# Kernel optimization log

Hardware: AMD Instinct MI355X
Metric: run time of the kernel (lower is better)

## Reference

```python
import jax, jax.numpy as jnp
import numpy as np

N = 100000      # nodes
F_IN = 256      # num_node_features
E = 1600000     # edges (before self-loops)
DIMS = [F_IN, 128, 100, 32, 2]  # GCNConv layer widths


def _glorot(key, fan_in, fan_out):
    s = jnp.sqrt(6.0 / (fan_in + fan_out))
    return jax.random.uniform(key, (fan_in, fan_out), jnp.float32, -s, s)


def setup_inputs() -> dict:
    key = jax.random.key(0)
    ks = jax.random.split(key, 10)
    x = jax.random.normal(ks[0], (N, F_IN), jnp.float32)
    edge_index = jax.random.randint(ks[1], (2, E), 0, N, jnp.int32)
    inp = {"x": x, "edge_index": edge_index}
    for i in range(4):
        inp[f"W{i+1}"] = _glorot(ks[2 + 2 * i], DIMS[i], DIMS[i + 1])
        inp[f"b{i+1}"] = jnp.zeros((DIMS[i + 1],), jnp.float32)
    return inp


def reference(x, edge_index, W1, b1, W2, b2, W3, b3, W4, b4):
    n = x.shape[0]
    loops = jnp.arange(n, dtype=edge_index.dtype)
    src = jnp.concatenate([edge_index[0], loops])  # [E+N]
    dst = jnp.concatenate([edge_index[1], loops])
    # symmetric normalization: deg^-1/2[src] * deg^-1/2[dst] (self-loops included)
    deg = jax.ops.segment_sum(jnp.ones_like(src, x.dtype), dst, num_segments=n)
    dis = jax.lax.rsqrt(jnp.maximum(deg, 1.0))
    norm = (dis[src] * dis[dst])[:, None]  # [E+N, 1]

    def conv(h, W, b):
        h = h @ W                                      # [N, out]
        msg = h[src] * norm                            # gather + scale [E+N, out]
        return jax.ops.segment_sum(msg, dst, num_segments=n) + b

    h = jax.nn.leaky_relu(conv(x, W1, b1), negative_slope=0.1)
    h = jax.nn.leaky_relu(conv(h, W2, b2), negative_slope=0.1)
    h = jax.nn.leaky_relu(conv(h, W3, b3), negative_slope=0.1)
    h = conv(h, W4, b4)
    return jax.nn.softmax(h, axis=-1)
```

## Files before the change

kernel.cpp:

```cpp
#include <hip/hip_runtime.h>
#include <math.h>


typedef unsigned short ushort_t;
typedef unsigned int   uint_t;
typedef short  bf16x8 __attribute__((ext_vector_type(8)));
typedef float  f32x4  __attribute__((ext_vector_type(4)));

#define BKT_SHIFT 8
#define BKT_CAP   5120
#define BIN_CHUNK 4096

__device__ __forceinline__ ushort_t f2bf(float f) {
    union { float f; uint_t u; } v; v.f = f;
    uint_t u = v.u;
    u += 0x7fffu + ((u >> 16) & 1u);
    return (ushort_t)(u >> 16);
}
__device__ __forceinline__ float bflo(uint_t u) {
    union { uint_t q; float f; } v; v.q = u << 16; return v.f;
}
__device__ __forceinline__ float bfhi(uint_t u) {
    union { uint_t q; float f; } v; v.q = u & 0xffff0000u; return v.f;
}


__global__ __launch_bounds__(256) void bin_kernel(const int* __restrict__ srcArr,
                                                  const int* __restrict__ dstArr,
                                                  int* __restrict__ bkt_cursor,
                                                  uint2* __restrict__ staging,
                                                  int E, int nb) {
    __shared__ int hist[512];
    __shared__ int base[512];
    for (int b = threadIdx.x; b < 512; b += 256) hist[b] = 0;
    __syncthreads();
    const int e0 = blockIdx.x * BIN_CHUNK;
    #pragma unroll 4
    for (int k = 0; k < BIN_CHUNK / 256; ++k) {
        int e = e0 + k * 256 + threadIdx.x;
        if (e < E) atomicAdd(&hist[dstArr[e] >> BKT_SHIFT], 1);
    }
    __syncthreads();
    for (int b = threadIdx.x; b < nb; b += 256) {
        int h = hist[b];
        base[b] = h ? atomicAdd(&bkt_cursor[b], h) : 0;
    }
    __syncthreads();
    for (int b = threadIdx.x; b < 512; b += 256) hist[b] = 0;
    __syncthreads();
    #pragma unroll 4
    for (int k = 0; k < BIN_CHUNK / 256; ++k) {
        int e = e0 + k * 256 + threadIdx.x;
        if (e < E) {
            int s = srcArr[e], d = dstArr[e];
            int b = d >> BKT_SHIFT;
            int p = atomicAdd(&hist[b], 1);
            int idx = base[b] + p;
            if (idx < BKT_CAP)
                staging[(size_t)b * BKT_CAP + idx] = make_uint2((uint_t)s, (uint_t)d);
        }
    }
}

__global__ __launch_bounds__(256) void deg_from_staging_kernel(const uint2* __restrict__ staging,
                                                               const int* __restrict__ bkt_cursor,
                                                               int* __restrict__ degi,
                                                               float* __restrict__ dis, int n) {
    __shared__ int cur[256];
    const int b  = blockIdx.x;
    const int lo = b << BKT_SHIFT;
    const int nl = min(256, n - lo);
    cur[threadIdx.x] = 0;
    __syncthreads();
    int cnt = min(bkt_cursor[b], BKT_CAP);
    for (int e = threadIdx.x; e < cnt; e += 256) {
        uint2 p = staging[(size_t)b * BKT_CAP + e];
        atomicAdd(&cur[(int)p.y - lo], 1);
    }
    __syncthreads();
    if ((int)threadIdx.x < nl) {
        int d = cur[threadIdx.x];
        degi[lo + threadIdx.x] = d;
        dis[lo + threadIdx.x] = rsqrtf((float)(d + 1));
    }
}

__global__ void scan_block_kernel(const int* __restrict__ degi, int* __restrict__ row_excl,
                                  int* __restrict__ bsums, int n) {
    __shared__ int buf[1024];
    int i = blockIdx.x * 1024 + threadIdx.x;
    int v = (i < n) ? degi[i] : 0;
    buf[threadIdx.x] = v;
    __syncthreads();
    for (int off = 1; off < 1024; off <<= 1) {
        int t = (threadIdx.x >= (unsigned)off) ? buf[threadIdx.x - off] : 0;
        __syncthreads();
        buf[threadIdx.x] += t;
        __syncthreads();
    }
    if (i < n) row_excl[i] = buf[threadIdx.x] - v;
    if (threadIdx.x == 1023) bsums[blockIdx.x] = buf[1023];
}

__global__ void scan_sums_kernel(int* __restrict__ bsums, int nb) {
    __shared__ int buf[128];
    int v = ((int)threadIdx.x < nb) ? bsums[threadIdx.x] : 0;
    buf[threadIdx.x] = v;
    __syncthreads();
    for (int off = 1; off < 128; off <<= 1) {
        int t = (threadIdx.x >= (unsigned)off) ? buf[threadIdx.x - off] : 0;
        __syncthreads();
        buf[threadIdx.x] += t;
        __syncthreads();
    }
    if ((int)threadIdx.x < nb) bsums[threadIdx.x] = buf[threadIdx.x] - v;
    if (threadIdx.x == 0) bsums[nb] = buf[127];
}

__global__ void scan_add_kernel(int* __restrict__ row_start, const int* __restrict__ bsums,
                                int n, int nb) {
    int i = blockIdx.x * blockDim.x + threadIdx.x;
    if (i < n) row_start[i] += bsums[i >> 10];
    else if (i == n) row_start[n] = bsums[nb];
}

__global__ __launch_bounds__(256) void csr_build_kernel(const uint2* __restrict__ staging,
                                                        const int* __restrict__ bkt_cursor,
                                                        const int* __restrict__ row_start,
                                                        int* __restrict__ csr_src, int n) {
    __shared__ int rs[257];
    __shared__ int cur[256];
    __shared__ int seg[BKT_CAP];
    const int b  = blockIdx.x;
    const int lo = b << BKT_SHIFT;
    const int nl = min(256, n - lo);
    if ((int)threadIdx.x <= nl) rs[threadIdx.x] = row_start[lo + threadIdx.x];
    cur[threadIdx.x] = 0;
    __syncthreads();
    const int sbase = rs[0];
    int cnt = min(bkt_cursor[b], BKT_CAP);
    for (int e = threadIdx.x; e < cnt; e += 256) {
        uint2 p = staging[(size_t)b * BKT_CAP + e];
        int ln = (int)p.y - lo;
        int q  = atomicAdd(&cur[ln], 1);
        seg[(rs[ln] - sbase) + q] = (int)p.x;
    }
    __syncthreads();
    for (int i = threadIdx.x; i < cnt; i += 256) csr_src[sbase + i] = seg[i];
}

__global__ void wt_all_kernel(const float* __restrict__ W1, const float* __restrict__ W2,
                              const float* __restrict__ W3,
                              ushort_t* __restrict__ Wt1, ushort_t* __restrict__ Wt2,
                              ushort_t* __restrict__ Wt3) {
    int idx = blockIdx.x * blockDim.x + threadIdx.x;
    if (idx < 32768) {
        int nn = idx >> 8, k = idx & 255;
        Wt1[idx] = f2bf(W1[(size_t)k * 128 + nn]);
    } else if (idx < 49152) {
        int j = idx - 32768;
        int nn = j >> 7, k = j & 127;
        float v = (nn < 100) ? W2[(size_t)k * 100 + nn] : 0.f;
        Wt2[j] = f2bf(v);
    } else if (idx < 57344) {
        int j = idx - 49152;
        int nn = j >> 7, k = j & 127;
        float v = (k < 100 && nn < 32) ? W3[(size_t)k * 32 + nn] : 0.f;
        Wt3[j] = f2bf(v);
    }
}

template <bool A_FP32, int NFR>
__global__ __launch_bounds__(256) void mfma_gemm(const void* __restrict__ Av,
                                                 const ushort_t* __restrict__ Bt,
                                                 ushort_t* __restrict__ C,
                                                 const float* __restrict__ dis,
                                                 int M, int K, int lda, int ldb,
                                                 int ldc, int nstore) {
    constexpr int BN = NFR * 32;
    __shared__ __attribute__((aligned(16))) ushort_t As[128][72];
    __shared__ __attribute__((aligned(16))) ushort_t Bs[BN][72];

    const int t    = threadIdx.x;
    const int lane = t & 63;
    const int w    = t >> 6;
    const int wm   = w >> 1, wn = w & 1;
    const int m0   = blockIdx.x * 128;
    const int n0   = blockIdx.y * BN;

    f32x4 acc[4][NFR];
    #pragma unroll
    for (int mi = 0; mi < 4; ++mi)
        #pragma unroll
        for (int ni = 0; ni < NFR; ++ni) acc[mi][ni] = (f32x4){0.f, 0.f, 0.f, 0.f};

    const int srow = t >> 3;
    const int scol = (t & 7) * 8;

    for (int k0 = 0; k0 < K; k0 += 64) {
        #pragma unroll
        for (int it = 0; it < 4; ++it) {
            int r = srow + it * 32;
            int gm = m0 + r;
            bf16x8 v = {0, 0, 0, 0, 0, 0, 0, 0};
            if (gm < M) {
                if (A_FP32) {
                    const float* A = (const float*)Av;
                    const float4 f0 = *(const float4*)(A + (size_t)gm * lda + k0 + scol);
                    const float4 f1 = *(const float4*)(A + (size_t)gm * lda + k0 + scol + 4);
                    ushort_t o[8] = { f2bf(f0.x), f2bf(f0.y), f2bf(f0.z), f2bf(f0.w),
                                      f2bf(f1.x), f2bf(f1.y), f2bf(f1.z), f2bf(f1.w) };
                    v = *(const bf16x8*)o;
                } else {
                    const ushort_t* A = (const ushort_t*)Av;
                    v = *(const bf16x8*)(A + (size_t)gm * lda + k0 + scol);
                }
            }
            *(bf16x8*)&As[r][scol] = v;
        }
        #pragma unroll
        for (int it = 0; it < BN / 32; ++it) {
            int r = srow + it * 32;
            bf16x8 v = *(const bf16x8*)(Bt + (size_t)(n0 + r) * ldb + k0 + scol);
            *(bf16x8*)&Bs[r][scol] = v;
        }
        __syncthreads();
        #pragma unroll
        for (int kk = 0; kk < 2; ++kk) {
            bf16x8 af[4], bfr[NFR];
            const int kc = kk * 32 + (lane >> 4) * 8;
            #pragma unroll
            for (int mi = 0; mi < 4; ++mi)
                af[mi] = *(const bf16x8*)&As[wm * 64 + mi * 16 + (lane & 15)][kc];
            #pragma unroll
            for (int ni = 0; ni < NFR; ++ni)
                bfr[ni] = *(const bf16x8*)&Bs[wn * (BN / 2) + ni * 16 + (lane & 15)][kc];
            #pragma unroll
            for (int mi = 0; mi < 4; ++mi)
                #pragma unroll
                for (int ni = 0; ni < NFR; ++ni)
                    acc[mi][ni] = __builtin_amdgcn_mfma_f32_16x16x32_bf16(
                        af[mi], bfr[ni], acc[mi][ni], 0, 0, 0);
        }
        __syncthreads();
    }

    #pragma unroll
    for (int mi = 0; mi < 4; ++mi)
        #pragma unroll
        for (int r = 0; r < 4; ++r) {
            int gm = m0 + wm * 64 + mi * 16 + (lane >> 4) * 4 + r;
            if (gm >= M) continue;
            float d = dis[gm];
            #pragma unroll
            for (int ni = 0; ni < NFR; ++ni) {
                int gn = n0 + wn * (BN / 2) + ni * 16 + (lane & 15);
                if (gn < nstore)
                    C[(size_t)gm * ldc + gn] = f2bf(acc[mi][ni][r] * d);
            }
        }
}

template <int F>
__global__ void aggregate128_kernel(const ushort_t* __restrict__ h, const int* __restrict__ row_start,
                                    const int* __restrict__ csr_src,
                                    const float* __restrict__ dis, const float* __restrict__ bias,
                                    ushort_t* __restrict__ out, int n) {
    int wid  = threadIdx.x >> 6;
    int lane = threadIdx.x & 63;
    int node = blockIdx.x * 4 + wid;
    if (node >= n) return;
    const int q  = lane >> 4;
    const int fb = (lane & 15) * 8;
    float a[8];
    #pragma unroll
    for (int j = 0; j < 8; ++j) a[j] = 0.f;

    int i = row_start[node], end = row_start[node + 1];

#define ACC8(U)                                                     \
    do {                                                            \
        a[0] += bflo((U).x); a[1] += bfhi((U).x);                   \
        a[2] += bflo((U).y); a[3] += bfhi((U).y);                   \
        a[4] += bflo((U).z); a[5] += bfhi((U).z);                   \
        a[6] += bflo((U).w); a[7] += bfhi((U).w);                   \
    } while (0)

    #pragma unroll 2
    for (; i + 8 <= end; i += 8) {
        int sA = csr_src[i + q];
        int sB = csr_src[i + 4 + q];
        uint4 u = *(const uint4*)(h + (size_t)sA * 128 + fb);
        uint4 v = *(const uint4*)(h + (size_t)sB * 128 + fb);
        ACC8(u);
        ACC8(v);
    }
    int r = end - i;
    if (r > 0) {
        if (q < r) {
            int sA = csr_src[i + q];
            uint4 u = *(const uint4*)(h + (size_t)sA * 128 + fb);
            ACC8(u);
        }
        if (q + 4 < r) {
            int sB = csr_src[i + 4 + q];
            uint4 v = *(const uint4*)(h + (size_t)sB * 128 + fb);
            ACC8(v);
        }
    }
#undef ACC8

    #pragma unroll
    for (int j = 0; j < 8; ++j) {
        a[j] += __shfl_xor(a[j], 16);
        a[j] += __shfl_xor(a[j], 32);
    }

    if (q == 0) {
        uint4 su = *(const uint4*)(h + (size_t)node * 128 + fb);
        a[0] += bflo(su.x); a[1] += bfhi(su.x);
        a[2] += bflo(su.y); a[3] += bfhi(su.y);
        a[4] += bflo(su.z); a[5] += bfhi(su.z);
        a[6] += bflo(su.w); a[7] += bfhi(su.w);
        float dn = dis[node];
        #pragma unroll
        for (int j = 0; j < 8; ++j) {
            float b = (fb + j < F) ? bias[fb + j] : 0.f;
            float v = a[j] * dn + b;
            v = (v > 0.f) ? v : 0.1f * v;
            if (fb + j >= F) v = 0.f;
            a[j] = v;
        }
        uint4 o;
        o.x = (uint_t)f2bf(a[0]) | ((uint_t)f2bf(a[1]) << 16);
        o.y = (uint_t)f2bf(a[2]) | ((uint_t)f2bf(a[3]) << 16);
        o.z = (uint_t)f2bf(a[4]) | ((uint_t)f2bf(a[5]) << 16);
        o.w = (uint_t)f2bf(a[6]) | ((uint_t)f2bf(a[7]) << 16);
        *(uint4*)(out + (size_t)node * 128 + fb) = o;
    }
}

__global__ void aggregate32_kernel(const ushort_t* __restrict__ h, const int* __restrict__ row_start,
                                   const int* __restrict__ csr_src,
                                   const float* __restrict__ dis, const float* __restrict__ bias,
                                   ushort_t* __restrict__ out, int n) {
    int lane16 = threadIdx.x & 15;
    int node = blockIdx.x * (blockDim.x >> 4) + (threadIdx.x >> 4);
    if (node >= n) return;
    const int f0 = 2 * lane16;
    uint_t v = *(const uint_t*)(h + (size_t)node * 32 + f0);
    float acc0 = bflo(v);
    float acc1 = bfhi(v);
    int i = row_start[node], end = row_start[node + 1];
    for (; i + 4 <= end; i += 4) {
        int s0 = csr_src[i], s1 = csr_src[i + 1], s2 = csr_src[i + 2], s3 = csr_src[i + 3];
        uint_t u0 = *(const uint_t*)(h + (size_t)s0 * 32 + f0);
        uint_t u1 = *(const uint_t*)(h + (size_t)s1 * 32 + f0);
        uint_t u2 = *(const uint_t*)(h + (size_t)s2 * 32 + f0);
        uint_t u3 = *(const uint_t*)(h + (size_t)s3 * 32 + f0);
        acc0 += bflo(u0) + bflo(u1) + bflo(u2) + bflo(u3);
        acc1 += bfhi(u0) + bfhi(u1) + bfhi(u2) + bfhi(u3);
    }
    for (; i < end; ++i) {
        int s = csr_src[i];
        uint_t u = *(const uint_t*)(h + (size_t)s * 32 + f0);
        acc0 += bflo(u); acc1 += bfhi(u);
    }
    float dn = dis[node];
    acc0 = acc0 * dn + bias[f0];
    acc1 = acc1 * dn + bias[f0 + 1];
    acc0 = (acc0 > 0.f) ? acc0 : 0.1f * acc0;
    acc1 = (acc1 > 0.f) ? acc1 : 0.1f * acc1;
    uint_t o = (uint_t)f2bf(acc0) | ((uint_t)f2bf(acc1) << 16);
    *(uint_t*)(out + (size_t)node * 32 + f0) = o;
}

__global__ void gemm32x2_kernel(const ushort_t* __restrict__ H, const float* __restrict__ W4,
                                const float* __restrict__ dis, float* __restrict__ C, int n) {
    int node = blockIdx.x * blockDim.x + threadIdx.x;
    if (node >= n) return;
    const uint_t* row = (const uint_t*)(H + (size_t)node * 32);
    float a0 = 0.f, a1 = 0.f;
    #pragma unroll
    for (int k2 = 0; k2 < 16; ++k2) {
        uint_t u = row[k2];
        float x0 = bflo(u), x1 = bfhi(u);
        int k = 2 * k2;
        a0 += x0 * W4[k * 2]     + x1 * W4[(k + 1) * 2];
        a1 += x0 * W4[k * 2 + 1] + x1 * W4[(k + 1) * 2 + 1];
    }
    float d = dis[node];
    C[2 * (size_t)node]     = a0 * d;
    C[2 * (size_t)node + 1] = a1 * d;
}

__global__ void aggregate2_softmax_kernel(const float* __restrict__ h, const int* __restrict__ row_start,
                                          const int* __restrict__ csr_src,
                                          const float* __restrict__ dis, const float* __restrict__ bias,
                                          float* __restrict__ out, int n) {
    int node = blockIdx.x * blockDim.x + threadIdx.x;
    if (node >= n) return;
    float a0 = h[2 * (size_t)node];
    float a1 = h[2 * (size_t)node + 1];
    int beg = row_start[node], end = row_start[node + 1];
    for (int i = beg; i < end; ++i) {
        int s = csr_src[i];
        a0 += h[2 * (size_t)s];
        a1 += h[2 * (size_t)s + 1];
    }
    float dn = dis[node];
    a0 = a0 * dn + bias[0];
    a1 = a1 * dn + bias[1];
    float m  = fmaxf(a0, a1);
    float e0 = expf(a0 - m), e1 = expf(a1 - m);
    float inv = 1.f / (e0 + e1);
    out[2 * (size_t)node]     = e0 * inv;
    out[2 * (size_t)node + 1] = e1 * inv;
}


extern "C" void kernel_launch(void* const* d_in, const int* in_sizes, int n_in,
                              void* d_out, int out_size, void* d_ws, size_t ws_size,
                              hipStream_t stream) {
    const float* x  = (const float*)d_in[0];
    const int*   ei = (const int*)d_in[1];
    const float* W1 = (const float*)d_in[2];
    const float* b1 = (const float*)d_in[3];
    const float* W2 = (const float*)d_in[4];
    const float* b2 = (const float*)d_in[5];
    const float* W3 = (const float*)d_in[6];
    const float* b3 = (const float*)d_in[7];
    const float* W4 = (const float*)d_in[8];
    const float* b4 = (const float*)d_in[9];

    const int N = in_sizes[0] / 256;
    const int E = in_sizes[1] / 2;
    const int* srcA = ei;
    const int* dstA = ei + E;
    const int nbkt = (N + 255) >> BKT_SHIFT;

    char* ws = (char*)d_ws;
    size_t off = 0;
    auto alloc = [&](size_t bytes) {
        void* p = ws + off;
        off = (off + bytes + 255) & ~(size_t)255;
        return p;
    };
    int*      degi       = (int*)alloc((size_t)N * 4);
    float*    dis        = (float*)alloc((size_t)N * 4);
    int*      row_start  = (int*)alloc((size_t)(N + 1) * 4);
    int*      bsums      = (int*)alloc(512 * 4);
    int*      bkt_cursor = (int*)alloc((size_t)nbkt * 4);
    int*      csr_src    = (int*)alloc((size_t)E * 4);
    uint2*    staging    = (uint2*)alloc((size_t)nbkt * BKT_CAP * 8);
    ushort_t* bufA       = (ushort_t*)alloc((size_t)N * 128 * 2);
    ushort_t* bufB       = (ushort_t*)alloc((size_t)N * 128 * 2);
    float*    C4         = (float*)alloc((size_t)N * 2 * 4);
    ushort_t* Wt1        = (ushort_t*)alloc((size_t)128 * 256 * 2);
    ushort_t* Wt2        = (ushort_t*)alloc((size_t)128 * 128 * 2);
    ushort_t* Wt3        = (ushort_t*)alloc((size_t)64 * 128 * 2);
    (void)ws_size;

    hipMemsetAsync(bkt_cursor, 0, (size_t)nbkt * 4, stream);

    bin_kernel<<<(E + BIN_CHUNK - 1) / BIN_CHUNK, 256, 0, stream>>>(
        srcA, dstA, bkt_cursor, staging, E, nbkt);
    deg_from_staging_kernel<<<nbkt, 256, 0, stream>>>(staging, bkt_cursor, degi, dis, N);
    const int nb = (N + 1023) >> 10;
    scan_block_kernel<<<nb, 1024, 0, stream>>>(degi, row_start, bsums, N);
    scan_sums_kernel<<<1, 128, 0, stream>>>(bsums, nb);
    scan_add_kernel<<<(N + 256) / 256, 256, 0, stream>>>(row_start, bsums, N, nb);
    csr_build_kernel<<<nbkt, 256, 0, stream>>>(staging, bkt_cursor, row_start, csr_src, N);

    wt_all_kernel<<<(57344 + 255) / 256, 256, 0, stream>>>(W1, W2, W3, Wt1, Wt2, Wt3);

    const int gx = (N + 127) / 128;
    const int aggBlocks128 = (N + 3) / 4;
    const int aggBlocks32  = (N + 15) / 16;

    mfma_gemm<true, 4><<<dim3(gx, 1), 256, 0, stream>>>(x, Wt1, bufA, dis, N, 256, 256, 256, 128, 128);
    aggregate128_kernel<128><<<aggBlocks128, 256, 0, stream>>>(
        bufA, row_start, csr_src, dis, b1, bufB, N);
    mfma_gemm<false, 4><<<dim3(gx, 1), 256, 0, stream>>>(bufB, Wt2, bufA, dis, N, 128, 128, 128, 128, 128);
    aggregate128_kernel<100><<<aggBlocks128, 256, 0, stream>>>(
        bufA, row_start, csr_src, dis, b2, bufB, N);
    mfma_gemm<false, 2><<<dim3(gx, 1), 256, 0, stream>>>(bufB, Wt3, bufA, dis, N, 128, 128, 128, 32, 32);
    aggregate32_kernel<<<aggBlocks32, 256, 0, stream>>>(
        bufA, row_start, csr_src, dis, b3, bufB, N);
    gemm32x2_kernel<<<(N + 255) / 256, 256, 0, stream>>>(bufB, W4, dis, C4, N);
    aggregate2_softmax_kernel<<<(N + 255) / 256, 256, 0, stream>>>(
        C4, row_start, csr_src, dis, b4, (float*)d_out, N);
}
```

Baseline: 321.7 us.

## Replace LDS-tiled MFMA GEMM with direct-register GEMM without shared memory

The shared-memory tiled GEMM is replaced by a kernel in which each wave loads its A rows and all of B straight from global memory into MFMA operand registers. Each wave owns 32 rows and the full output width, with the K loop fully unrolled at compile time. This removes LDS staging and the two __syncthreads per K step. In exchange, B (the small weight matrix) is re-read from global or cache by every wave, and the A loads are strided rather than coalesced through LDS.

```diff
diff --git a/kernel.cpp b/kernel.cpp
--- a/kernel.cpp
+++ b/kernel.cpp
@@ -170,91 +170,72 @@
     }
 }
 
-template <bool A_FP32, int NFR>
-__global__ __launch_bounds__(256) void mfma_gemm(const void* __restrict__ Av,
-                                                 const ushort_t* __restrict__ Bt,
-                                                 ushort_t* __restrict__ C,
-                                                 const float* __restrict__ dis,
-                                                 int M, int K, int lda, int ldb,
-                                                 int ldc, int nstore) {
-    constexpr int BN = NFR * 32;
-    __shared__ __attribute__((aligned(16))) ushort_t As[128][72];
-    __shared__ __attribute__((aligned(16))) ushort_t Bs[BN][72];
-
-    const int t    = threadIdx.x;
-    const int lane = t & 63;
-    const int w    = t >> 6;
-    const int wm   = w >> 1, wn = w & 1;
-    const int m0   = blockIdx.x * 128;
-    const int n0   = blockIdx.y * BN;
-
-    f32x4 acc[4][NFR];
-    #pragma unroll
-    for (int mi = 0; mi < 4; ++mi)
+template <bool A_FP32, int NFR, int KT>
+__global__ __launch_bounds__(256) void gemm_direct(const void* __restrict__ Av,
+                                                   const ushort_t* __restrict__ Bt,
+                                                   ushort_t* __restrict__ C,
+                                                   const float* __restrict__ dis,
+                                                   int M, int lda, int ldb,
+                                                   int ldc, int nstore) {
+    const int lane = threadIdx.x & 63;
+    const int w    = threadIdx.x >> 6;
+    const int row0 = blockIdx.x * 128 + w * 32;
+    const int rsel = lane & 15;
+    const int kq   = (lane >> 4) * 8;
+
+    f32x4 acc[2][NFR];
+    #pragma unroll
+    for (int mi = 0; mi < 2; ++mi)
         #pragma unroll
         for (int ni = 0; ni < NFR; ++ni) acc[mi][ni] = (f32x4){0.f, 0.f, 0.f, 0.f};
 
-    const int srow = t >> 3;
-    const int scol = (t & 7) * 8;
-
-    for (int k0 = 0; k0 < K; k0 += 64) {
-        #pragma unroll
-        for (int it = 0; it < 4; ++it) {
-            int r = srow + it * 32;
-            int gm = m0 + r;
+    const int gm0 = row0 + rsel;
+    const int gm1 = row0 + 16 + rsel;
+
+    #pragma unroll
+    for (int k0 = 0; k0 < KT; k0 += 32) {
+        bf16x8 af[2];
+        #pragma unroll
+        for (int mi = 0; mi < 2; ++mi) {
+            int gm = mi ? gm1 : gm0;
             bf16x8 v = {0, 0, 0, 0, 0, 0, 0, 0};
             if (gm < M) {
                 if (A_FP32) {
                     const float* A = (const float*)Av;
-                    const float4 f0 = *(const float4*)(A + (size_t)gm * lda + k0 + scol);
-                    const float4 f1 = *(const float4*)(A + (size_t)gm * lda + k0 + scol + 4);
+                    const float4 f0 = *(const float4*)(A + (size_t)gm * lda + k0 + kq);
+                    const float4 f1 = *(const float4*)(A + (size_t)gm * lda + k0 + kq + 4);
                     ushort_t o[8] = { f2bf(f0.x), f2bf(f0.y), f2bf(f0.z), f2bf(f0.w),
                                       f2bf(f1.x), f2bf(f1.y), f2bf(f1.z), f2bf(f1.w) };
                     v = *(const bf16x8*)o;
                 } else {
                     const ushort_t* A = (const ushort_t*)Av;
-                    v = *(const bf16x8*)(A + (size_t)gm * lda + k0 + scol);
+                    v = *(const bf16x8*)(A + (size_t)gm * lda + k0 + kq);
                 }
             }
-            *(bf16x8*)&As[r][scol] = v;
-        }
-        #pragma unroll
-        for (int it = 0; it < BN / 32; ++it) {
-            int r = srow + it * 32;
-            bf16x8 v = *(const bf16x8*)(Bt + (size_t)(n0 + r) * ldb + k0 + scol);
-            *(bf16x8*)&Bs[r][scol] = v;
-        }
-        __syncthreads();
-        #pragma unroll
-        for (int kk = 0; kk < 2; ++kk) {
-            bf16x8 af[4], bfr[NFR];
-            const int kc = kk * 32 + (lane >> 4) * 8;
-            #pragma unroll
-            for (int mi = 0; mi < 4; ++mi)
-                af[mi] = *(const bf16x8*)&As[wm * 64 + mi * 16 + (lane & 15)][kc];
+            af[mi] = v;
+        }
+        bf16x8 bfr[NFR];
+        #pragma unroll
+        for (int ni = 0; ni < NFR; ++ni)
+            bfr[ni] = *(const bf16x8*)(Bt + (size_t)(ni * 16 + rsel) * ldb + k0 + kq);
+        #pragma unroll
+        for (int mi = 0; mi < 2; ++mi)
             #pragma unroll
             for (int ni = 0; ni < NFR; ++ni)
-                bfr[ni] = *(const bf16x8*)&Bs[wn * (BN / 2) + ni * 16 + (lane & 15)][kc];
-            #pragma unroll
-            for (int mi = 0; mi < 4; ++mi)
-                #pragma unroll
-                for (int ni = 0; ni < NFR; ++ni)
-                    acc[mi][ni] = __builtin_amdgcn_mfma_f32_16x16x32_bf16(
-                        af[mi], bfr[ni], acc[mi][ni], 0, 0, 0);
-        }
-        __syncthreads();
-    }
-
-    #pragma unroll
-    for (int mi = 0; mi < 4; ++mi)
+                acc[mi][ni] = __builtin_amdgcn_mfma_f32_16x16x32_bf16(
+                    af[mi], bfr[ni], acc[mi][ni], 0, 0, 0);
+    }
+
+    #pragma unroll
+    for (int mi = 0; mi < 2; ++mi)
         #pragma unroll
         for (int r = 0; r < 4; ++r) {
-            int gm = m0 + wm * 64 + mi * 16 + (lane >> 4) * 4 + r;
+            int gm = row0 + mi * 16 + (lane >> 4) * 4 + r;
             if (gm >= M) continue;
             float d = dis[gm];
             #pragma unroll
             for (int ni = 0; ni < NFR; ++ni) {
-                int gn = n0 + wn * (BN / 2) + ni * 16 + (lane & 15);
+                int gn = ni * 16 + rsel;
                 if (gn < nstore)
                     C[(size_t)gm * ldc + gn] = f2bf(acc[mi][ni][r] * d);
             }
@@ -478,13 +459,13 @@
     const int aggBlocks128 = (N + 3) / 4;
     const int aggBlocks32  = (N + 15) / 16;
 
-    mfma_gemm<true, 4><<<dim3(gx, 1), 256, 0, stream>>>(x, Wt1, bufA, dis, N, 256, 256, 256, 128, 128);
+    gemm_direct<true, 8, 256><<<gx, 256, 0, stream>>>(x, Wt1, bufA, dis, N, 256, 256, 128, 128);
     aggregate128_kernel<128><<<aggBlocks128, 256, 0, stream>>>(
         bufA, row_start, csr_src, dis, b1, bufB, N);
-    mfma_gemm<false, 4><<<dim3(gx, 1), 256, 0, stream>>>(bufB, Wt2, bufA, dis, N, 128, 128, 128, 128, 128);
+    gemm_direct<false, 8, 128><<<gx, 256, 0, stream>>>(bufB, Wt2, bufA, dis, N, 128, 128, 128, 128);
     aggregate128_kernel<100><<<aggBlocks128, 256, 0, stream>>>(
         bufA, row_start, csr_src, dis, b2, bufB, N);
-    mfma_gemm<false, 2><<<dim3(gx, 1), 256, 0, stream>>>(bufB, Wt3, bufA, dis, N, 128, 128, 128, 32, 32);
+    gemm_direct<false, 2, 128><<<gx, 256, 0, stream>>>(bufB, Wt3, bufA, dis, N, 128, 128, 32, 32);
     aggregate32_kernel<<<aggBlocks32, 256, 0, stream>>>(
         bufA, row_start, csr_src, dis, b3, bufB, N);
     gemm32x2_kernel<<<(N + 255) / 256, 256, 0, stream>>>(bufB, W4, dis, C4, N);
```

After: 350.8 us. 1.09x slower.

## Pre-cast x to bf16, shrink GEMM M-tile, swap MFMA operands for vector stores

Applied to the files above, without the earlier changes.

Adds a separate kernel that casts the fp32 input features to a bf16 buffer before the first GEMM, so the GEMM no longer converts on load. The GEMM M-tile is halved from 128 to 64 rows, which doubles the block count and lowers register use. The MFMA operands are swapped so each lane holds four consecutive output columns and can write them as one packed 8-byte store. The third layer now uses a 32-wide tile instead of 64. The cost is an extra pass over x, reading 100 MB of fp32 and writing 50 MB of bf16, plus a larger workspace.

```diff
diff --git a/kernel.cpp b/kernel.cpp
--- a/kernel.cpp
+++ b/kernel.cpp
@@ -147,6 +147,20 @@
     }
     __syncthreads();
     for (int i = threadIdx.x; i < cnt; i += 256) csr_src[sbase + i] = seg[i];
+}
+
+
+__global__ void cast_bf16_kernel(const float* __restrict__ in, ushort_t* __restrict__ out, int n8) {
+    int i = blockIdx.x * blockDim.x + threadIdx.x;
+    if (i >= n8) return;
+    const float4 f0 = ((const float4*)in)[2 * i];
+    const float4 f1 = ((const float4*)in)[2 * i + 1];
+    uint4 o;
+    o.x = (uint_t)f2bf(f0.x) | ((uint_t)f2bf(f0.y) << 16);
+    o.y = (uint_t)f2bf(f0.z) | ((uint_t)f2bf(f0.w) << 16);
+    o.z = (uint_t)f2bf(f1.x) | ((uint_t)f2bf(f1.y) << 16);
+    o.w = (uint_t)f2bf(f1.z) | ((uint_t)f2bf(f1.w) << 16);
+    ((uint4*)out)[i] = o;
 }
 
 __global__ void wt_all_kernel(const float* __restrict__ W1, const float* __restrict__ W2,
@@ -170,27 +184,27 @@
     }
 }
 
-template <bool A_FP32, int NFR>
-__global__ __launch_bounds__(256) void mfma_gemm(const void* __restrict__ Av,
+template <int NFR>
+__global__ __launch_bounds__(256) void gemm_tile(const ushort_t* __restrict__ A,
                                                  const ushort_t* __restrict__ Bt,
                                                  ushort_t* __restrict__ C,
                                                  const float* __restrict__ dis,
-                                                 int M, int K, int lda, int ldb,
-                                                 int ldc, int nstore) {
+                                                 int M, int K, int lda, int ldb, int ldc) {
     constexpr int BN = NFR * 32;
-    __shared__ __attribute__((aligned(16))) ushort_t As[128][72];
+    __shared__ __attribute__((aligned(16))) ushort_t As[64][72];
     __shared__ __attribute__((aligned(16))) ushort_t Bs[BN][72];
 
     const int t    = threadIdx.x;
     const int lane = t & 63;
     const int w    = t >> 6;
     const int wm   = w >> 1, wn = w & 1;
-    const int m0   = blockIdx.x * 128;
-    const int n0   = blockIdx.y * BN;
-
-    f32x4 acc[4][NFR];
+    const int m0   = blockIdx.x * 64;
+    const int rsel = lane & 15;
+    const int q    = lane >> 4;
+
+    f32x4 acc[2][NFR];
     #pragma unroll
-    for (int mi = 0; mi < 4; ++mi)
+    for (int mi = 0; mi < 2; ++mi)
         #pragma unroll
         for (int ni = 0; ni < NFR; ++ni) acc[mi][ni] = (f32x4){0.f, 0.f, 0.f, 0.f};
 
@@ -199,66 +213,53 @@
 
     for (int k0 = 0; k0 < K; k0 += 64) {
         #pragma unroll
-        for (int it = 0; it < 4; ++it) {
+        for (int it = 0; it < 2; ++it) {
             int r = srow + it * 32;
             int gm = m0 + r;
             bf16x8 v = {0, 0, 0, 0, 0, 0, 0, 0};
-            if (gm < M) {
-                if (A_FP32) {
-                    const float* A = (const float*)Av;
-                    const float4 f0 = *(const float4*)(A + (size_t)gm * lda + k0 + scol);
-                    const float4 f1 = *(const float4*)(A + (size_t)gm * lda + k0 + scol + 4);
-                    ushort_t o[8] = { f2bf(f0.x), f2bf(f0.y), f2bf(f0.z), f2bf(f0.w),
-                                      f2bf(f1.x), f2bf(f1.y), f2bf(f1.z), f2bf(f1.w) };
-                    v = *(const bf16x8*)o;
-                } else {
-                    const ushort_t* A = (const ushort_t*)Av;
-                    v = *(const bf16x8*)(A + (size_t)gm * lda + k0 + scol);
-                }
-            }
+            if (gm < M) v = *(const bf16x8*)(A + (size_t)gm * lda + k0 + scol);
             *(bf16x8*)&As[r][scol] = v;
         }
         #pragma unroll
         for (int it = 0; it < BN / 32; ++it) {
             int r = srow + it * 32;
-            bf16x8 v = *(const bf16x8*)(Bt + (size_t)(n0 + r) * ldb + k0 + scol);
+            bf16x8 v = *(const bf16x8*)(Bt + (size_t)r * ldb + k0 + scol);
             *(bf16x8*)&Bs[r][scol] = v;
         }
         __syncthreads();
         #pragma unroll
-        for (int kk = 0; kk < 2; ++kk) {
-            bf16x8 af[4], bfr[NFR];
-            const int kc = kk * 32 + (lane >> 4) * 8;
+        for (int ks = 0; ks < 2; ++ks) {
+            const int kc = ks * 32 + q * 8;
+            bf16x8 af[2], bfr[NFR];
             #pragma unroll
-            for (int mi = 0; mi < 4; ++mi)
-                af[mi] = *(const bf16x8*)&As[wm * 64 + mi * 16 + (lane & 15)][kc];
+            for (int mi = 0; mi < 2; ++mi)
+                af[mi] = *(const bf16x8*)&As[wm * 32 + mi * 16 + rsel][kc];
             #pragma unroll
             for (int ni = 0; ni < NFR; ++ni)
-                bfr[ni] = *(const bf16x8*)&Bs[wn * (BN / 2) + ni * 16 + (lane & 15)][kc];
+                bfr[ni] = *(const bf16x8*)&Bs[wn * (BN / 2) + ni * 16 + rsel][kc];
             #pragma unroll
-            for (int mi = 0; mi < 4; ++mi)
+            for (int mi = 0; mi < 2; ++mi)
                 #pragma unroll
                 for (int ni = 0; ni < NFR; ++ni)
                     acc[mi][ni] = __builtin_amdgcn_mfma_f32_16x16x32_bf16(
-                        af[mi], bfr[ni], acc[mi][ni], 0, 0, 0);
+                        bfr[ni], af[mi], acc[mi][ni], 0, 0, 0);
         }
         __syncthreads();
     }
 
     #pragma unroll
-    for (int mi = 0; mi < 4; ++mi)
-        #pragma unroll
-        for (int r = 0; r < 4; ++r) {
-            int gm = m0 + wm * 64 + mi * 16 + (lane >> 4) * 4 + r;
-            if (gm >= M) continue;
-            float d = dis[gm];
-            #pragma unroll
-            for (int ni = 0; ni < NFR; ++ni) {
-                int gn = n0 + wn * (BN / 2) + ni * 16 + (lane & 15);
-                if (gn < nstore)
-                    C[(size_t)gm * ldc + gn] = f2bf(acc[mi][ni][r] * d);
-            }
-        }
+    for (int mi = 0; mi < 2; ++mi) {
+        const int gm = m0 + wm * 32 + mi * 16 + rsel;
+        if (gm >= M) continue;
+        const float d = dis[gm];
+        #pragma unroll
+        for (int ni = 0; ni < NFR; ++ni) {
+            uint2 o;
+            o.x = (uint_t)f2bf(acc[mi][ni][0] * d) | ((uint_t)f2bf(acc[mi][ni][1] * d) << 16);
+            o.y = (uint_t)f2bf(acc[mi][ni][2] * d) | ((uint_t)f2bf(acc[mi][ni][3] * d) << 16);
+            *(uint2*)(C + (size_t)gm * ldc + wn * (BN / 2) + ni * 16 + q * 4) = o;
+        }
+    }
 }
 
 template <int F>
@@ -453,6 +454,7 @@
     int*      bkt_cursor = (int*)alloc((size_t)nbkt * 4);
     int*      csr_src    = (int*)alloc((size_t)E * 4);
     uint2*    staging    = (uint2*)alloc((size_t)nbkt * BKT_CAP * 8);
+    ushort_t* xb         = (ushort_t*)alloc((size_t)N * 256 * 2);
     ushort_t* bufA       = (ushort_t*)alloc((size_t)N * 128 * 2);
     ushort_t* bufB       = (ushort_t*)alloc((size_t)N * 128 * 2);
     float*    C4         = (float*)alloc((size_t)N * 2 * 4);
@@ -473,18 +475,20 @@
     csr_build_kernel<<<nbkt, 256, 0, stream>>>(staging, bkt_cursor, row_start, csr_src, N);
 
     wt_all_kernel<<<(57344 + 255) / 256, 256, 0, stream>>>(W1, W2, W3, Wt1, Wt2, Wt3);
-
-    const int gx = (N + 127) / 128;
+    const int n8 = N * 32;
+    cast_bf16_kernel<<<(n8 + 255) / 256, 256, 0, stream>>>(x, xb, n8);
+
+    const int gx = (N + 63) / 64;
     const int aggBlocks128 = (N + 3) / 4;
     const int aggBlocks32  = (N + 15) / 16;
 
-    mfma_gemm<true, 4><<<dim3(gx, 1), 256, 0, stream>>>(x, Wt1, bufA, dis, N, 256, 256, 256, 128, 128);
+    gemm_tile<4><<<gx, 256, 0, stream>>>(xb, Wt1, bufA, dis, N, 256, 256, 256, 128);
     aggregate128_kernel<128><<<aggBlocks128, 256, 0, stream>>>(
         bufA, row_start, csr_src, dis, b1, bufB, N);
-    mfma_gemm<false, 4><<<dim3(gx, 1), 256, 0, stream>>>(bufB, Wt2, bufA, dis, N, 128, 128, 128, 128, 128);
+    gemm_tile<4><<<gx, 256, 0, stream>>>(bufB, Wt2, bufA, dis, N, 128, 128, 128, 128);
     aggregate128_kernel<100><<<aggBlocks128, 256, 0, stream>>>(
         bufA, row_start, csr_src, dis, b2, bufB, N);
-    mfma_gemm<false, 2><<<dim3(gx, 1), 256, 0, stream>>>(bufB, Wt3, bufA, dis, N, 128, 128, 128, 32, 32);
+    gemm_tile<1><<<gx, 256, 0, stream>>>(bufB, Wt3, bufA, dis, N, 128, 128, 128, 32);
     aggregate32_kernel<<<aggBlocks32, 256, 0, stream>>>(
         bufA, row_start, csr_src, dis, b3, bufB, N);
     gemm32x2_kernel<<<(N + 255) / 256, 256, 0, stream>>>(bufB, W4, dis, C4, N);
```

Measured after the change: 317.4 us. Within noise of the previous version (-1.3%).
